# Performance work log

Measured on AMD Instinct MI355X. Metric: run time of the kernel, lower is better.

The kernel has to match this reference:

```python
import jax, jax.numpy as jnp
import numpy as np

B, N, D, H, E = 32, 512, 512, 8, 4
HD = D // H
EPS = 1e-3  # keras LayerNormalization default epsilon
NEG = -1e9  # keras Softmax masking additive constant


def _ln(x, g, b):
    m = jnp.mean(x, axis=-1, keepdims=True)
    v = jnp.mean(jnp.square(x - m), axis=-1, keepdims=True)
    return (x - m) * jax.lax.rsqrt(v + EPS) * g + b


def setup_inputs() -> dict:
    key = jax.random.key(0)
    ks = jax.random.split(key, 16)
    s = 0.02
    return {
        "x": jax.random.normal(ks[0], (B, N, D), jnp.float32),
        "mask": jax.random.randint(ks[1], (B, 1, N, N), 0, 2) > 0,
        "interaction": jax.random.normal(ks[2], (B, N, N, H), jnp.float32),
        "w_qkv": jax.random.normal(ks[3], (D, 3 * D), jnp.float32) * s,
        "b_qkv": jnp.zeros((3 * D,), jnp.float32),
        "w_out": jax.random.normal(ks[4], (D, D), jnp.float32) * s,
        "b_out": jnp.zeros((D,), jnp.float32),
        "w1": jax.random.normal(ks[5], (D, E * D), jnp.float32) * s,
        "b1": jnp.zeros((E * D,), jnp.float32),
        "w2": jax.random.normal(ks[6], (E * D, D), jnp.float32) * s,
        "b2": jnp.zeros((D,), jnp.float32),
        "g_pre": jnp.ones((D,), jnp.float32), "be_pre": jnp.zeros((D,), jnp.float32),
        "g_post": jnp.ones((D,), jnp.float32), "be_post": jnp.zeros((D,), jnp.float32),
        "g_ffn": jnp.ones((D,), jnp.float32), "be_ffn": jnp.zeros((D,), jnp.float32),
        "g_mid": jnp.ones((E * D,), jnp.float32), "be_mid": jnp.zeros((E * D,), jnp.float32),
    }


def reference(x, mask, interaction, w_qkv, b_qkv, w_out, b_out, w1, b1, w2, b2,
              g_pre, be_pre, g_post, be_post, g_ffn, be_ffn, g_mid, be_mid):
    # pre-LN MHSA
    h = _ln(x, g_pre, be_pre)
    qkv = h @ w_qkv + b_qkv                           # [B,N,3D]
    qkv = qkv.reshape(B, N, 3, H, HD)
    q, k, v = (jnp.transpose(qkv[:, :, i], (0, 2, 1, 3)) for i in range(3))  # [B,H,N,HD]
    scores = jnp.einsum('bhnd,bhmd->bhnm', q, k) / np.sqrt(HD).astype(np.float32)
    scores = scores + jnp.transpose(interaction, (0, 3, 1, 2))  # per-head additive bias
    scores = scores + (1.0 - mask.astype(scores.dtype)) * NEG   # keras Softmax mask semantics
    attn = jax.nn.softmax(scores, axis=-1)
    o = jnp.einsum('bhnm,bhmd->bhnd', attn, v)
    o = jnp.transpose(o, (0, 2, 1, 3)).reshape(B, N, D)
    o = o @ w_out + b_out
    attended = _ln(o, g_post, be_post) + x            # post-MHSA LN then residual
    # FFN with mid-LN
    f = _ln(attended, g_ffn, be_ffn)
    f = jax.nn.gelu(f @ w1 + b1, approximate=False)
    f = _ln(f, g_mid, be_mid)
    f = f @ w2 + b2
    return f + attended
```

## Files before the change

### kernel.cpp

```cpp
#include <hip/hip_runtime.h>
#include <hip/hip_bf16.h>
#include <math.h>

constexpr int CB = 32, CN = 512, CD = 512, CH = 8, CHD = 64;
constexpr float LN_EPS = 1e-3f;

typedef _Float16 half8 __attribute__((ext_vector_type(8)));
typedef float f32x4 __attribute__((ext_vector_type(4)));

__device__ __forceinline__ void async16(const void* g, void* l) {
    __builtin_amdgcn_global_load_lds((const __attribute__((address_space(1))) void*)g,
                                     (__attribute__((address_space(3))) void*)l, 16, 0, 0);
}

__global__ __launch_bounds__(256) void transpose_f16(const float* __restrict__ in,
                                                     _Float16* __restrict__ out,
                                                     int K, int N) {
    __shared__ float t[32][33];
    const int tx = threadIdx.x % 32, ty = threadIdx.x / 32;
    const int n0 = blockIdx.x * 32, k0 = blockIdx.y * 32;
#pragma unroll
    for (int i = 0; i < 4; ++i)
        t[ty + i * 8][tx] = in[(size_t)(k0 + ty + i * 8) * N + n0 + tx];
    __syncthreads();
#pragma unroll
    for (int i = 0; i < 4; ++i)
        out[(size_t)(n0 + ty + i * 8) * K + k0 + tx] = (_Float16)t[tx][ty + i * 8];
}

template<int WIDTH, bool IN_F16, bool OUT_F16, bool ADDRES>
__global__ __launch_bounds__(256) void ln2_kernel(const void* __restrict__ in_,
        const float* __restrict__ g, const float* __restrict__ be,
        const float* __restrict__ res, void* __restrict__ out_) {
    constexpr int NPL = WIDTH / 64;
    const int row = blockIdx.x * 4 + (threadIdx.x >> 6);
    const int lane = threadIdx.x & 63;
    const int c0 = lane * NPL;
    float v[NPL];
    if (IN_F16) {
        const _Float16* p = (const _Float16*)in_ + (size_t)row * WIDTH + c0;
#pragma unroll
        for (int i = 0; i < NPL / 8; ++i) {
            half8 u = *(const half8*)(p + i * 8);
#pragma unroll
            for (int j = 0; j < 8; ++j) v[i * 8 + j] = (float)u[j];
        }
    } else {
        const float* p = (const float*)in_ + (size_t)row * WIDTH + c0;
#pragma unroll
        for (int i = 0; i < NPL / 4; ++i) {
            float4 u = *(const float4*)(p + i * 4);
            v[i * 4 + 0] = u.x; v[i * 4 + 1] = u.y; v[i * 4 + 2] = u.z; v[i * 4 + 3] = u.w;
        }
    }
    float s1 = 0.f, s2 = 0.f;
#pragma unroll
    for (int i = 0; i < NPL; ++i) { s1 += v[i]; s2 += v[i] * v[i]; }
#pragma unroll
    for (int off = 1; off < 64; off <<= 1) { s1 += __shfl_xor(s1, off); s2 += __shfl_xor(s2, off); }
    const float mean = s1 * (1.0f / WIDTH);
    const float var = s2 * (1.0f / WIDTH) - mean * mean;
    const float rstd = rsqrtf(var + LN_EPS);

    float ov[NPL];
#pragma unroll
    for (int i = 0; i < NPL / 4; ++i) {
        float4 gv = *(const float4*)(g + c0 + i * 4);
        float4 bv = *(const float4*)(be + c0 + i * 4);
        ov[i * 4 + 0] = (v[i * 4 + 0] - mean) * rstd * gv.x + bv.x;
        ov[i * 4 + 1] = (v[i * 4 + 1] - mean) * rstd * gv.y + bv.y;
        ov[i * 4 + 2] = (v[i * 4 + 2] - mean) * rstd * gv.z + bv.z;
        ov[i * 4 + 3] = (v[i * 4 + 3] - mean) * rstd * gv.w + bv.w;
    }
    if (ADDRES) {
        const float* rp = res + (size_t)row * WIDTH + c0;
#pragma unroll
        for (int i = 0; i < NPL / 4; ++i) {
            float4 rv = *(const float4*)(rp + i * 4);
            ov[i * 4 + 0] += rv.x; ov[i * 4 + 1] += rv.y; ov[i * 4 + 2] += rv.z; ov[i * 4 + 3] += rv.w;
        }
    }
    if (OUT_F16) {
        _Float16* po = (_Float16*)out_ + (size_t)row * WIDTH + c0;
#pragma unroll
        for (int i = 0; i < NPL / 8; ++i) {
            half8 hv;
#pragma unroll
            for (int j = 0; j < 8; ++j) hv[j] = (_Float16)ov[i * 8 + j];
            *(half8*)(po + i * 8) = hv;
        }
    } else {
        float* po = (float*)out_ + (size_t)row * WIDTH + c0;
#pragma unroll
        for (int i = 0; i < NPL / 4; ++i) {
            float4 w = make_float4(ov[i * 4 + 0], ov[i * 4 + 1], ov[i * 4 + 2], ov[i * 4 + 3]);
            *(float4*)(po + i * 4) = w;
        }
    }
}

__global__ __launch_bounds__(256) void ln_post_ffn(const _Float16* __restrict__ o2,
        const float* __restrict__ x,
        const float* __restrict__ g_post, const float* __restrict__ be_post,
        const float* __restrict__ g_ffn, const float* __restrict__ be_ffn,
        float* __restrict__ attended, _Float16* __restrict__ f) {
    constexpr int NPL = 8;
    const int row = blockIdx.x * 4 + (threadIdx.x >> 6);
    const int lane = threadIdx.x & 63;
    const int c0 = lane * NPL;
    float v[NPL], xv[NPL];
    {
        half8 u = *(const half8*)(o2 + (size_t)row * CD + c0);
#pragma unroll
        for (int j = 0; j < 8; ++j) v[j] = (float)u[j];
        float4 a = *(const float4*)(x + (size_t)row * CD + c0);
        float4 b = *(const float4*)(x + (size_t)row * CD + c0 + 4);
        xv[0] = a.x; xv[1] = a.y; xv[2] = a.z; xv[3] = a.w;
        xv[4] = b.x; xv[5] = b.y; xv[6] = b.z; xv[7] = b.w;
    }
    float s1 = 0.f, s2 = 0.f;
#pragma unroll
    for (int i = 0; i < NPL; ++i) { s1 += v[i]; s2 += v[i] * v[i]; }
#pragma unroll
    for (int off = 1; off < 64; off <<= 1) { s1 += __shfl_xor(s1, off); s2 += __shfl_xor(s2, off); }
    float mean = s1 * (1.0f / CD);
    float rstd = rsqrtf(s2 * (1.0f / CD) - mean * mean + LN_EPS);
    float av[NPL];
#pragma unroll
    for (int i = 0; i < NPL; ++i)
        av[i] = (v[i] - mean) * rstd * g_post[c0 + i] + be_post[c0 + i] + xv[i];
    {
        float4 w0 = make_float4(av[0], av[1], av[2], av[3]);
        float4 w1 = make_float4(av[4], av[5], av[6], av[7]);
        *(float4*)(attended + (size_t)row * CD + c0) = w0;
        *(float4*)(attended + (size_t)row * CD + c0 + 4) = w1;
    }
    s1 = 0.f; s2 = 0.f;
#pragma unroll
    for (int i = 0; i < NPL; ++i) { s1 += av[i]; s2 += av[i] * av[i]; }
#pragma unroll
    for (int off = 1; off < 64; off <<= 1) { s1 += __shfl_xor(s1, off); s2 += __shfl_xor(s2, off); }
    mean = s1 * (1.0f / CD);
    rstd = rsqrtf(s2 * (1.0f / CD) - mean * mean + LN_EPS);
    half8 hv;
#pragma unroll
    for (int i = 0; i < NPL; ++i)
        hv[i] = (_Float16)((av[i] - mean) * rstd * g_ffn[c0 + i] + be_ffn[c0 + i]);
    *(half8*)(f + (size_t)row * CD + c0) = hv;
}

template<bool GELU, bool RES, bool OUT_F16>
__global__ __launch_bounds__(256) void gemm_f16(const _Float16* __restrict__ A,
        const _Float16* __restrict__ Wt, const float* __restrict__ bias,
        const float* __restrict__ res, void* __restrict__ Cout,
        int M, int N, int K) {
    __shared__ __align__(16) char As[16384];
    __shared__ __align__(16) char Bs[16384];
    const int tid = threadIdx.x;
    const int nbx = N >> 7;
    const int nwg = (M >> 7) * nbx;
    int gb = blockIdx.x;
    gb = (gb & 7) * (nwg >> 3) + (gb >> 3);
    const int by = gb / nbx, bx = gb % nbx;

    const int lane = tid & 63;
    const int wv = tid >> 6;
    const int rsub = lane >> 3;
    const int slot = lane & 7;
    const int chunk = slot ^ rsub;
    const _Float16* Abase = A + (size_t)(by * 128) * K + chunk * 8;
    const _Float16* Bbase = Wt + (size_t)(bx * 128) * K + chunk * 8;

    const int wm = wv >> 1, wn = wv & 1;
    const int lrow = lane & 15;
    const int lk = lane >> 4;
    const int xorv = lane & 7;
    const int aRowB = (wm * 64 + lrow) * 128;
    const int bRowB = (wn * 64 + lrow) * 128;

    f32x4 acc[4][4] = {};

    for (int k0 = 0; k0 < K; k0 += 64) {
#pragma unroll
        for (int t = 0; t < 4; ++t) {
            const int rowb = t * 32 + wv * 8;
            async16(Abase + (size_t)(rowb + rsub) * K + k0, As + rowb * 128);
            async16(Bbase + (size_t)(rowb + rsub) * K + k0, Bs + rowb * 128);
        }
        __syncthreads();
#pragma unroll
        for (int kk = 0; kk < 2; ++kk) {
            const int sa = ((kk * 4 + lk) ^ xorv) << 4;
            half8 af[4], bf[4];
#pragma unroll
            for (int mi = 0; mi < 4; ++mi) af[mi] = *(const half8*)(As + aRowB + mi * 2048 + sa);
#pragma unroll
            for (int ni = 0; ni < 4; ++ni) bf[ni] = *(const half8*)(Bs + bRowB + ni * 2048 + sa);
#pragma unroll
            for (int mi = 0; mi < 4; ++mi)
#pragma unroll
                for (int ni = 0; ni < 4; ++ni)
                    acc[mi][ni] = __builtin_amdgcn_mfma_f32_16x16x32_f16(af[mi], bf[ni], acc[mi][ni], 0, 0, 0);
        }
        __syncthreads();
    }

    const int lr4 = (lane >> 4) * 4;
    const int lc = lane & 15;
#pragma unroll
    for (int ni = 0; ni < 4; ++ni) {
        const int colg = bx * 128 + wn * 64 + ni * 16 + lc;
        const float bv = bias[colg];
#pragma unroll
        for (int mi = 0; mi < 4; ++mi) {
            const int rowg = by * 128 + wm * 64 + mi * 16 + lr4;
#pragma unroll
            for (int r = 0; r < 4; ++r) {
                float v = acc[mi][ni][r] + bv;
                if (GELU) v = 0.5f * v * (1.0f + erff(v * 0.70710678118654752440f));
                if (RES) v += res[(size_t)(rowg + r) * N + colg];
                if (OUT_F16) ((_Float16*)Cout)[(size_t)(rowg + r) * N + colg] = (_Float16)v;
                else ((float*)Cout)[(size_t)(rowg + r) * N + colg] = v;
            }
        }
    }
}

__global__ __launch_bounds__(256) void attn_mfma(
        const _Float16* __restrict__ qkv, const float* __restrict__ inter,
        const int* __restrict__ mask, _Float16* __restrict__ o) {
    const int bid = blockIdx.x;
    const int xcd = bid & 7;
    const int s = bid >> 3;
    const int h = s & 7;
    const int qt = (s >> 3) & 7;
    const int b = (s >> 6) * 8 + xcd;
    const int tid = threadIdx.x;
    const int lane = tid & 63;
    const int w = tid >> 6;
    const int l15 = lane & 15, l4 = lane >> 4;

    __shared__ __align__(16) char Qs[8192];
    __shared__ __align__(16) char Ks[8192];
    __shared__ __align__(16) char Vt[8192];
    __shared__ __align__(16) char Ps[8192];

    constexpr size_t QKVROW = 1536;
    {
        const _Float16* Qg = qkv + (size_t)(b * CN + qt * 64) * QKVROW + h * 64;
#pragma unroll
        for (int p = 0; p < 2; ++p) {
            const int f = tid + 256 * p;
            const int r = f >> 3, c = f & 7;
            half8 v = *(const half8*)(Qg + (size_t)r * QKVROW + c * 8);
            *(half8*)(Qs + r * 128 + ((c ^ (r & 7)) << 4)) = v;
        }
    }

    f32x4 acc_o[4] = {};
    float m_run[4] = {-3e38f, -3e38f, -3e38f, -3e38f};
    float l_run[4] = {0.f, 0.f, 0.f, 0.f};

    const int qg0 = qt * 64 + w * 16 + l4 * 4;
    const float* interB[4];
    const int* maskB[4];
#pragma unroll
    for (int r = 0; r < 4; ++r) {
        interB[r] = inter + ((size_t)(b * CN + qg0 + r) * CN) * CH + h;
        maskB[r]  = mask + (size_t)(b * CN + qg0 + r) * CN;
    }

    for (int mt = 0; mt < 8; ++mt) {
        __syncthreads();
        const _Float16* Kg = qkv + (size_t)(b * CN + mt * 64) * QKVROW + 512 + h * 64;
        const _Float16* Vg = Kg + 512;
#pragma unroll
        for (int p = 0; p < 2; ++p) {
            const int f = tid + 256 * p;
            const int r = f >> 3, c = f & 7;
            half8 kv = *(const half8*)(Kg + (size_t)r * QKVROW + c * 8);
            *(half8*)(Ks + r * 128 + ((c ^ (r & 7)) << 4)) = kv;
        }
#pragma unroll
        for (int p = 0; p < 2; ++p) {
            const int f = tid + 256 * p;
            const int m = f >> 3, dc = f & 7;
            half8 vv = *(const half8*)(Vg + (size_t)m * QKVROW + dc * 8);
            const int mc = m >> 3, mo = m & 7;
#pragma unroll
            for (int j = 0; j < 8; ++j) {
                const int d = dc * 8 + j;
                *(_Float16*)(Vt + d * 128 + ((mc ^ (d & 7)) << 4) + mo * 2) = vv[j];
            }
        }
        float iv[4][4];
#pragma unroll
        for (int r = 0; r < 4; ++r)
#pragma unroll
            for (int mi = 0; mi < 4; ++mi) {
                const int m = mt * 64 + mi * 16 + l15;
                const float bvv = interB[r][(size_t)m * CH];
                iv[r][mi] = bvv + (maskB[r][m] ? 0.f : -1e9f);
            }
        __syncthreads();

        f32x4 acc_s[4] = {};
#pragma unroll
        for (int step = 0; step < 2; ++step) {
            const int qrow = w * 16 + l15;
            const int ch = step * 4 + l4;
            half8 aq = *(const half8*)(Qs + qrow * 128 + ((ch ^ (qrow & 7)) << 4));
#pragma unroll
            for (int mi = 0; mi < 4; ++mi) {
                const int mrow = mi * 16 + l15;
                half8 bk = *(const half8*)(Ks + mrow * 128 + ((ch ^ (mrow & 7)) << 4));
                acc_s[mi] = __builtin_amdgcn_mfma_f32_16x16x32_f16(aq, bk, acc_s[mi], 0, 0, 0);
            }
        }
#pragma unroll
        for (int r = 0; r < 4; ++r) {
            float pv[4];
            float rmax = -3e38f;
#pragma unroll
            for (int mi = 0; mi < 4; ++mi) {
                float sv = acc_s[mi][r] * 0.125f + iv[r][mi];
                pv[mi] = sv;
                rmax = fmaxf(rmax, sv);
            }
#pragma unroll
            for (int off = 1; off < 16; off <<= 1) rmax = fmaxf(rmax, __shfl_xor(rmax, off));
            const float nm = fmaxf(m_run[r], rmax);
            const float fac = __expf(m_run[r] - nm);
            m_run[r] = nm;
            float ps = 0.f;
#pragma unroll
            for (int mi = 0; mi < 4; ++mi) { float e = __expf(pv[mi] - nm); pv[mi] = e; ps += e; }
#pragma unroll
            for (int off = 1; off < 16; off <<= 1) ps += __shfl_xor(ps, off);
            l_run[r] = l_run[r] * fac + ps;
#pragma unroll
            for (int di = 0; di < 4; ++di) acc_o[di][r] *= fac;
            const int qrow = w * 16 + l4 * 4 + r;
#pragma unroll
            for (int mi = 0; mi < 4; ++mi) {
                const int m = mi * 16 + l15;
                *(_Float16*)(Ps + qrow * 128 + (((m >> 3) ^ (qrow & 7)) << 4) + (m & 7) * 2) = (_Float16)pv[mi];
            }
        }
#pragma unroll
        for (int step = 0; step < 2; ++step) {
            const int qrow = w * 16 + l15;
            const int ch = step * 4 + l4;
            half8 ap = *(const half8*)(Ps + qrow * 128 + ((ch ^ (qrow & 7)) << 4));
#pragma unroll
            for (int di = 0; di < 4; ++di) {
                const int drow = di * 16 + l15;
                half8 bv = *(const half8*)(Vt + drow * 128 + ((ch ^ (drow & 7)) << 4));
                acc_o[di] = __builtin_amdgcn_mfma_f32_16x16x32_f16(ap, bv, acc_o[di], 0, 0, 0);
            }
        }
    }
    _Float16* orow = o + (size_t)(b * CN + qt * 64 + w * 16 + l4 * 4) * CD + h * 64 + l15;
#pragma unroll
    for (int r = 0; r < 4; ++r) {
        const float inv = 1.0f / l_run[r];
#pragma unroll
        for (int di = 0; di < 4; ++di)
            orow[(size_t)r * CD + di * 16] = (_Float16)(acc_o[di][r] * inv);
    }
}

extern "C" void kernel_launch(void* const* d_in, const int* in_sizes, int n_in,
                              void* d_out, int out_size, void* d_ws, size_t ws_size,
                              hipStream_t stream) {
    const float* x      = (const float*)d_in[0];
    const int*   mask   = (const int*)d_in[1];
    const float* inter  = (const float*)d_in[2];
    const float* w_qkv  = (const float*)d_in[3];
    const float* b_qkv  = (const float*)d_in[4];
    const float* w_out  = (const float*)d_in[5];
    const float* b_out  = (const float*)d_in[6];
    const float* w1     = (const float*)d_in[7];
    const float* b1     = (const float*)d_in[8];
    const float* w2     = (const float*)d_in[9];
    const float* b2     = (const float*)d_in[10];
    const float* g_pre  = (const float*)d_in[11];
    const float* be_pre = (const float*)d_in[12];
    const float* g_post = (const float*)d_in[13];
    const float* be_post= (const float*)d_in[14];
    const float* g_ffn  = (const float*)d_in[15];
    const float* be_ffn = (const float*)d_in[16];
    const float* g_mid  = (const float*)d_in[17];
    const float* be_mid = (const float*)d_in[18];
    float* out = (float*)d_out;

    char* ws = (char*)d_ws;
    const size_t MB = 1ull << 20;
    _Float16* wt_qkv = (_Float16*)(ws + 0 * MB);
    _Float16* wt_out = (_Float16*)(ws + 2 * MB);
    _Float16* wt_w1  = (_Float16*)(ws + 3 * MB);
    _Float16* wt_w2  = (_Float16*)(ws + 5 * MB);
    float*    attended = (float*)(ws + 8 * MB);
    _Float16* o2h    = (_Float16*)(ws + 40 * MB);
    _Float16* f1b    = (_Float16*)(ws + 64 * MB);
    _Float16* qkvb   = (_Float16*)(ws + 128 * MB);
    _Float16* hb     = (_Float16*)(ws + 176 * MB);
    _Float16* ob     = (_Float16*)(ws + 192 * MB);
    _Float16* fb     = (_Float16*)(ws + 208 * MB);

    const int M = CB * CN;

    transpose_f16<<<dim3(1536 / 32, 512 / 32), 256, 0, stream>>>(w_qkv, wt_qkv, 512, 1536);
    transpose_f16<<<dim3(512 / 32, 512 / 32), 256, 0, stream>>>(w_out, wt_out, 512, 512);
    transpose_f16<<<dim3(2048 / 32, 512 / 32), 256, 0, stream>>>(w1, wt_w1, 512, 2048);
    transpose_f16<<<dim3(512 / 32, 2048 / 32), 256, 0, stream>>>(w2, wt_w2, 2048, 512);

    ln2_kernel<512, false, true, false><<<M / 4, 256, 0, stream>>>(x, g_pre, be_pre, nullptr, hb);
    gemm_f16<false, false, true><<<(M / 128) * (1536 / 128), 256, 0, stream>>>(
        hb, wt_qkv, b_qkv, nullptr, qkvb, M, 1536, 512);
    attn_mfma<<<CB * 8 * 8, 256, 0, stream>>>(qkvb, inter, mask, ob);
    gemm_f16<false, false, true><<<(M / 128) * (512 / 128), 256, 0, stream>>>(
        ob, wt_out, b_out, nullptr, o2h, M, 512, 512);
    ln_post_ffn<<<M / 4, 256, 0, stream>>>(o2h, x, g_post, be_post, g_ffn, be_ffn, attended, fb);
    gemm_f16<true, false, true><<<(M / 128) * (2048 / 128), 256, 0, stream>>>(
        fb, wt_w1, b1, nullptr, f1b, M, 2048, 512);
    ln2_kernel<2048, true, true, false><<<M / 4, 256, 0, stream>>>(f1b, g_mid, be_mid, nullptr, f1b);
    gemm_f16<false, true, false><<<(M / 128) * (512 / 128), 256, 0, stream>>>(
        f1b, wt_w2, b2, attended, out, M, 512, 2048);
}
```

Before: 460.9 us.

## Transpose attention score MFMA so each lane owns one query row for softmax

The QK^T MFMA operands are swapped so the score tile comes out transposed: each lane holds 16 key scores for a single query row. Row max and sum then need only two cross-lane shuffles instead of four per row, mask values are read as int4 vectors, and P is written to LDS as packed half4 stores instead of scalar halves. The running rescale factors and the final normalisers are broadcast back to the output layout with shuffles. s_setprio is also raised around the MFMA blocks in both the GEMM and attention kernels to favour matrix issue across waves.

```diff
diff --git a/kernel.cpp b/kernel.cpp
--- a/kernel.cpp
+++ b/kernel.cpp
@@ -6,6 +6,7 @@
 constexpr float LN_EPS = 1e-3f;
 
 typedef _Float16 half8 __attribute__((ext_vector_type(8)));
+typedef _Float16 half4v __attribute__((ext_vector_type(4)));
 typedef float f32x4 __attribute__((ext_vector_type(4)));
 
 __device__ __forceinline__ void async16(const void* g, void* l) {
@@ -196,11 +197,13 @@
             for (int mi = 0; mi < 4; ++mi) af[mi] = *(const half8*)(As + aRowB + mi * 2048 + sa);
 #pragma unroll
             for (int ni = 0; ni < 4; ++ni) bf[ni] = *(const half8*)(Bs + bRowB + ni * 2048 + sa);
+            __builtin_amdgcn_s_setprio(1);
 #pragma unroll
             for (int mi = 0; mi < 4; ++mi)
 #pragma unroll
                 for (int ni = 0; ni < 4; ++ni)
                     acc[mi][ni] = __builtin_amdgcn_mfma_f32_16x16x32_f16(af[mi], bf[ni], acc[mi][ni], 0, 0, 0);
+            __builtin_amdgcn_s_setprio(0);
         }
         __syncthreads();
     }
@@ -258,17 +261,11 @@
     }
 
     f32x4 acc_o[4] = {};
-    float m_run[4] = {-3e38f, -3e38f, -3e38f, -3e38f};
-    float l_run[4] = {0.f, 0.f, 0.f, 0.f};
-
-    const int qg0 = qt * 64 + w * 16 + l4 * 4;
-    const float* interB[4];
-    const int* maskB[4];
-#pragma unroll
-    for (int r = 0; r < 4; ++r) {
-        interB[r] = inter + ((size_t)(b * CN + qg0 + r) * CN) * CH + h;
-        maskB[r]  = mask + (size_t)(b * CN + qg0 + r) * CN;
-    }
+    float m_run = -3e38f, l_run = 0.f;
+
+    const int q_sm = qt * 64 + w * 16 + l15;
+    const float* interB = inter + ((size_t)(b * CN + q_sm) * CN) * CH + h;
+    const int* maskB = mask + (size_t)(b * CN + q_sm) * CN;
 
     for (int mt = 0; mt < 8; ++mt) {
         __syncthreads();
@@ -295,13 +292,14 @@
         }
         float iv[4][4];
 #pragma unroll
-        for (int r = 0; r < 4; ++r)
-#pragma unroll
-            for (int mi = 0; mi < 4; ++mi) {
-                const int m = mt * 64 + mi * 16 + l15;
-                const float bvv = interB[r][(size_t)m * CH];
-                iv[r][mi] = bvv + (maskB[r][m] ? 0.f : -1e9f);
-            }
+        for (int mi = 0; mi < 4; ++mi) {
+            const int m0 = mt * 64 + mi * 16 + l4 * 4;
+            const int4 mv = *(const int4*)(maskB + m0);
+            iv[mi][0] = interB[(size_t)(m0 + 0) * CH] + (mv.x ? 0.f : -1e9f);
+            iv[mi][1] = interB[(size_t)(m0 + 1) * CH] + (mv.y ? 0.f : -1e9f);
+            iv[mi][2] = interB[(size_t)(m0 + 2) * CH] + (mv.z ? 0.f : -1e9f);
+            iv[mi][3] = interB[(size_t)(m0 + 3) * CH] + (mv.w ? 0.f : -1e9f);
+        }
         __syncthreads();
 
         f32x4 acc_s[4] = {};
@@ -309,42 +307,59 @@
         for (int step = 0; step < 2; ++step) {
             const int qrow = w * 16 + l15;
             const int ch = step * 4 + l4;
-            half8 aq = *(const half8*)(Qs + qrow * 128 + ((ch ^ (qrow & 7)) << 4));
+            half8 bq = *(const half8*)(Qs + qrow * 128 + ((ch ^ (qrow & 7)) << 4));
+            __builtin_amdgcn_s_setprio(1);
 #pragma unroll
             for (int mi = 0; mi < 4; ++mi) {
                 const int mrow = mi * 16 + l15;
-                half8 bk = *(const half8*)(Ks + mrow * 128 + ((ch ^ (mrow & 7)) << 4));
-                acc_s[mi] = __builtin_amdgcn_mfma_f32_16x16x32_f16(aq, bk, acc_s[mi], 0, 0, 0);
-            }
-        }
-#pragma unroll
-        for (int r = 0; r < 4; ++r) {
-            float pv[4];
-            float rmax = -3e38f;
+                half8 ak = *(const half8*)(Ks + mrow * 128 + ((ch ^ (mrow & 7)) << 4));
+                acc_s[mi] = __builtin_amdgcn_mfma_f32_16x16x32_f16(ak, bq, acc_s[mi], 0, 0, 0);
+            }
+            __builtin_amdgcn_s_setprio(0);
+        }
+        float sv[4][4];
+        float rmax = -3e38f;
+#pragma unroll
+        for (int mi = 0; mi < 4; ++mi)
+#pragma unroll
+            for (int r = 0; r < 4; ++r) {
+                const float t = acc_s[mi][r] * 0.125f + iv[mi][r];
+                sv[mi][r] = t;
+                rmax = fmaxf(rmax, t);
+            }
+        rmax = fmaxf(rmax, __shfl_xor(rmax, 16));
+        rmax = fmaxf(rmax, __shfl_xor(rmax, 32));
+        const float nm = fmaxf(m_run, rmax);
+        const float fac = __expf(m_run - nm);
+        m_run = nm;
+        float ps = 0.f;
+#pragma unroll
+        for (int mi = 0; mi < 4; ++mi)
+#pragma unroll
+            for (int r = 0; r < 4; ++r) {
+                const float e = __expf(sv[mi][r] - nm);
+                sv[mi][r] = e;
+                ps += e;
+            }
+        ps += __shfl_xor(ps, 16);
+        ps += __shfl_xor(ps, 32);
+        l_run = l_run * fac + ps;
+        float facO[4];
+#pragma unroll
+        for (int r = 0; r < 4; ++r) facO[r] = __shfl(fac, l4 * 4 + r);
+#pragma unroll
+        for (int di = 0; di < 4; ++di)
+#pragma unroll
+            for (int r = 0; r < 4; ++r) acc_o[di][r] *= facO[r];
+        {
+            const int qloc = w * 16 + l15;
 #pragma unroll
             for (int mi = 0; mi < 4; ++mi) {
-                float sv = acc_s[mi][r] * 0.125f + iv[r][mi];
-                pv[mi] = sv;
-                rmax = fmaxf(rmax, sv);
-            }
-#pragma unroll
-            for (int off = 1; off < 16; off <<= 1) rmax = fmaxf(rmax, __shfl_xor(rmax, off));
-            const float nm = fmaxf(m_run[r], rmax);
-            const float fac = __expf(m_run[r] - nm);
-            m_run[r] = nm;
-            float ps = 0.f;
-#pragma unroll
-            for (int mi = 0; mi < 4; ++mi) { float e = __expf(pv[mi] - nm); pv[mi] = e; ps += e; }
-#pragma unroll
-            for (int off = 1; off < 16; off <<= 1) ps += __shfl_xor(ps, off);
-            l_run[r] = l_run[r] * fac + ps;
-#pragma unroll
-            for (int di = 0; di < 4; ++di) acc_o[di][r] *= fac;
-            const int qrow = w * 16 + l4 * 4 + r;
-#pragma unroll
-            for (int mi = 0; mi < 4; ++mi) {
-                const int m = mi * 16 + l15;
-                *(_Float16*)(Ps + qrow * 128 + (((m >> 3) ^ (qrow & 7)) << 4) + (m & 7) * 2) = (_Float16)pv[mi];
+                half4v pk;
+#pragma unroll
+                for (int r = 0; r < 4; ++r) pk[r] = (_Float16)sv[mi][r];
+                const int c16 = (mi * 2 + (l4 >> 1)) ^ (qloc & 7);
+                *(half4v*)(Ps + qloc * 128 + c16 * 16 + (l4 & 1) * 8) = pk;
             }
         }
 #pragma unroll
@@ -352,21 +367,25 @@
             const int qrow = w * 16 + l15;
             const int ch = step * 4 + l4;
             half8 ap = *(const half8*)(Ps + qrow * 128 + ((ch ^ (qrow & 7)) << 4));
+            __builtin_amdgcn_s_setprio(1);
 #pragma unroll
             for (int di = 0; di < 4; ++di) {
                 const int drow = di * 16 + l15;
                 half8 bv = *(const half8*)(Vt + drow * 128 + ((ch ^ (drow & 7)) << 4));
                 acc_o[di] = __builtin_amdgcn_mfma_f32_16x16x32_f16(ap, bv, acc_o[di], 0, 0, 0);
             }
-        }
-    }
+            __builtin_amdgcn_s_setprio(0);
+        }
+    }
+    float invO[4];
+#pragma unroll
+    for (int r = 0; r < 4; ++r) invO[r] = 1.0f / __shfl(l_run, l4 * 4 + r);
     _Float16* orow = o + (size_t)(b * CN + qt * 64 + w * 16 + l4 * 4) * CD + h * 64 + l15;
 #pragma unroll
     for (int r = 0; r < 4; ++r) {
-        const float inv = 1.0f / l_run[r];
 #pragma unroll
         for (int di = 0; di < 4; ++di)
-            orow[(size_t)r * CD + di * 16] = (_Float16)(acc_o[di][r] * inv);
+            orow[(size_t)r * CD + di * 16] = (_Float16)(acc_o[di][r] * invO[r]);
     }
 }
 
```

New measurement: 606.6 us. 1.32x slower.

## Double-buffer K/V tiles in attention with async LDS loads for K

Applied to the files above, without the earlier changes.

The attention kernel now keeps two K and two V shared-memory buffers. While the current key tile is computed, it prefetches the next one: K is copied straight into LDS with global_load_lds, and V is loaded into registers and written transposed after the softmax. This cuts the loop to one barrier per tile and hides global load latency behind the MFMA and softmax work. The mask select is moved to the point of use so the raw bias and mask loads can be issued early. The cost is twice the K/V LDS footprint, which may lower occupancy, plus more live registers for the V prefetch and the mask values.

```diff
diff --git a/kernel.cpp b/kernel.cpp
--- a/kernel.cpp
+++ b/kernel.cpp
@@ -241,11 +241,19 @@
     const int l15 = lane & 15, l4 = lane >> 4;
 
     __shared__ __align__(16) char Qs[8192];
-    __shared__ __align__(16) char Ks[8192];
-    __shared__ __align__(16) char Vt[8192];
     __shared__ __align__(16) char Ps[8192];
+    __shared__ __align__(16) char Kb[2][8192];
+    __shared__ __align__(16) char Vb[2][8192];
 
     constexpr size_t QKVROW = 1536;
+    const _Float16* kvK = qkv + (size_t)(b * CN) * QKVROW + 512 + h * 64;
+
+    const int rsub = lane >> 3, slot = lane & 7;
+    const int chunkK = slot ^ rsub;
+    const int w16 = w * 16;
+    const int vm0 = tid >> 3, vm1 = vm0 + 32;
+    const int vdc = tid & 7;
+
     {
         const _Float16* Qg = qkv + (size_t)(b * CN + qt * 64) * QKVROW + h * 64;
 #pragma unroll
@@ -256,12 +264,27 @@
             *(half8*)(Qs + r * 128 + ((c ^ (r & 7)) << 4)) = v;
         }
     }
+    {
+        const _Float16* Kg = kvK;
+        async16(Kg + (size_t)(w16 + rsub) * QKVROW + chunkK * 8, Kb[0] + w16 * 128);
+        async16(Kg + (size_t)(w16 + 8 + rsub) * QKVROW + chunkK * 8, Kb[0] + (w16 + 8) * 128);
+        const _Float16* Vg = Kg + 512;
+        half8 v0 = *(const half8*)(Vg + (size_t)vm0 * QKVROW + vdc * 8);
+        half8 v1 = *(const half8*)(Vg + (size_t)vm1 * QKVROW + vdc * 8);
+#pragma unroll
+        for (int j = 0; j < 8; ++j) {
+            const int d = vdc * 8 + j;
+            *(_Float16*)(Vb[0] + d * 128 + (((vm0 >> 3) ^ (d & 7)) << 4) + (vm0 & 7) * 2) = v0[j];
+            *(_Float16*)(Vb[0] + d * 128 + (((vm1 >> 3) ^ (d & 7)) << 4) + (vm1 & 7) * 2) = v1[j];
+        }
+    }
+    __syncthreads();
 
     f32x4 acc_o[4] = {};
     float m_run[4] = {-3e38f, -3e38f, -3e38f, -3e38f};
     float l_run[4] = {0.f, 0.f, 0.f, 0.f};
 
-    const int qg0 = qt * 64 + w * 16 + l4 * 4;
+    const int qg0 = qt * 64 + w16 + l4 * 4;
     const float* interB[4];
     const int* maskB[4];
 #pragma unroll
@@ -270,50 +293,38 @@
         maskB[r]  = mask + (size_t)(b * CN + qg0 + r) * CN;
     }
 
-    for (int mt = 0; mt < 8; ++mt) {
-        __syncthreads();
-        const _Float16* Kg = qkv + (size_t)(b * CN + mt * 64) * QKVROW + 512 + h * 64;
-        const _Float16* Vg = Kg + 512;
-#pragma unroll
-        for (int p = 0; p < 2; ++p) {
-            const int f = tid + 256 * p;
-            const int r = f >> 3, c = f & 7;
-            half8 kv = *(const half8*)(Kg + (size_t)r * QKVROW + c * 8);
-            *(half8*)(Ks + r * 128 + ((c ^ (r & 7)) << 4)) = kv;
-        }
-#pragma unroll
-        for (int p = 0; p < 2; ++p) {
-            const int f = tid + 256 * p;
-            const int m = f >> 3, dc = f & 7;
-            half8 vv = *(const half8*)(Vg + (size_t)m * QKVROW + dc * 8);
-            const int mc = m >> 3, mo = m & 7;
-#pragma unroll
-            for (int j = 0; j < 8; ++j) {
-                const int d = dc * 8 + j;
-                *(_Float16*)(Vt + d * 128 + ((mc ^ (d & 7)) << 4) + mo * 2) = vv[j];
-            }
+    auto body = [&](char* KC, char* VC, char* KN, char* VN, int mt) {
+        if (mt != 7) {
+            const _Float16* KgN = kvK + (size_t)((mt + 1) * 64) * QKVROW;
+            async16(KgN + (size_t)(w16 + rsub) * QKVROW + chunkK * 8, KN + w16 * 128);
+            async16(KgN + (size_t)(w16 + 8 + rsub) * QKVROW + chunkK * 8, KN + (w16 + 8) * 128);
+        }
+        half8 v0, v1;
+        if (mt != 7) {
+            const _Float16* VgN = kvK + (size_t)((mt + 1) * 64) * QKVROW + 512;
+            v0 = *(const half8*)(VgN + (size_t)vm0 * QKVROW + vdc * 8);
+            v1 = *(const half8*)(VgN + (size_t)vm1 * QKVROW + vdc * 8);
         }
         float iv[4][4];
+        int mvv[4][4];
 #pragma unroll
         for (int r = 0; r < 4; ++r)
 #pragma unroll
             for (int mi = 0; mi < 4; ++mi) {
                 const int m = mt * 64 + mi * 16 + l15;
-                const float bvv = interB[r][(size_t)m * CH];
-                iv[r][mi] = bvv + (maskB[r][m] ? 0.f : -1e9f);
-            }
-        __syncthreads();
-
+                iv[r][mi] = interB[r][(size_t)m * CH];
+                mvv[r][mi] = maskB[r][m];
+            }
         f32x4 acc_s[4] = {};
 #pragma unroll
         for (int step = 0; step < 2; ++step) {
-            const int qrow = w * 16 + l15;
+            const int qrow = w16 + l15;
             const int ch = step * 4 + l4;
             half8 aq = *(const half8*)(Qs + qrow * 128 + ((ch ^ (qrow & 7)) << 4));
 #pragma unroll
             for (int mi = 0; mi < 4; ++mi) {
                 const int mrow = mi * 16 + l15;
-                half8 bk = *(const half8*)(Ks + mrow * 128 + ((ch ^ (mrow & 7)) << 4));
+                half8 bk = *(const half8*)(KC + mrow * 128 + ((ch ^ (mrow & 7)) << 4));
                 acc_s[mi] = __builtin_amdgcn_mfma_f32_16x16x32_f16(aq, bk, acc_s[mi], 0, 0, 0);
             }
         }
@@ -323,7 +334,7 @@
             float rmax = -3e38f;
 #pragma unroll
             for (int mi = 0; mi < 4; ++mi) {
-                float sv = acc_s[mi][r] * 0.125f + iv[r][mi];
+                float sv = acc_s[mi][r] * 0.125f + iv[r][mi] + (mvv[r][mi] ? 0.f : -1e9f);
                 pv[mi] = sv;
                 rmax = fmaxf(rmax, sv);
             }
@@ -340,27 +351,42 @@
             l_run[r] = l_run[r] * fac + ps;
 #pragma unroll
             for (int di = 0; di < 4; ++di) acc_o[di][r] *= fac;
-            const int qrow = w * 16 + l4 * 4 + r;
+            const int qrow = w16 + l4 * 4 + r;
 #pragma unroll
             for (int mi = 0; mi < 4; ++mi) {
                 const int m = mi * 16 + l15;
                 *(_Float16*)(Ps + qrow * 128 + (((m >> 3) ^ (qrow & 7)) << 4) + (m & 7) * 2) = (_Float16)pv[mi];
             }
         }
+        if (mt != 7) {
+#pragma unroll
+            for (int j = 0; j < 8; ++j) {
+                const int d = vdc * 8 + j;
+                *(_Float16*)(VN + d * 128 + (((vm0 >> 3) ^ (d & 7)) << 4) + (vm0 & 7) * 2) = v0[j];
+                *(_Float16*)(VN + d * 128 + (((vm1 >> 3) ^ (d & 7)) << 4) + (vm1 & 7) * 2) = v1[j];
+            }
+        }
 #pragma unroll
         for (int step = 0; step < 2; ++step) {
-            const int qrow = w * 16 + l15;
+            const int qrow = w16 + l15;
             const int ch = step * 4 + l4;
             half8 ap = *(const half8*)(Ps + qrow * 128 + ((ch ^ (qrow & 7)) << 4));
 #pragma unroll
             for (int di = 0; di < 4; ++di) {
                 const int drow = di * 16 + l15;
-                half8 bv = *(const half8*)(Vt + drow * 128 + ((ch ^ (drow & 7)) << 4));
+                half8 bv = *(const half8*)(VC + drow * 128 + ((ch ^ (drow & 7)) << 4));
                 acc_o[di] = __builtin_amdgcn_mfma_f32_16x16x32_f16(ap, bv, acc_o[di], 0, 0, 0);
             }
         }
-    }
-    _Float16* orow = o + (size_t)(b * CN + qt * 64 + w * 16 + l4 * 4) * CD + h * 64 + l15;
+        __syncthreads();
+    };
+
+    for (int it = 0; it < 4; ++it) {
+        body(Kb[0], Vb[0], Kb[1], Vb[1], it * 2);
+        body(Kb[1], Vb[1], Kb[0], Vb[0], it * 2 + 1);
+    }
+
+    _Float16* orow = o + (size_t)(b * CN + qt * 64 + w16 + l4 * 4) * CD + h * 64 + l15;
 #pragma unroll
     for (int r = 0; r < 4; ++r) {
         const float inv = 1.0f / l_run[r];
```

After: 470.8 us. 1.02x slower.

## Process four heads per attention block with vectorized bias loads

Applied to the files above, without the earlier changes.

Restructures the attention kernel so each block handles four heads for one query tile. The per-head additive bias is read as a float4 across heads in one coalesced access, and mask reads are shared across those heads, cutting redundant global traffic on the large interaction tensor. Q is held in registers pre-scaled by the softmax scale, K tiles are loaded via async global-to-LDS, and the bias+mask are stored in fp16 with a smaller mask constant. This raises register and LDS use and reduces precision of the bias term.

```diff
diff --git a/kernel.cpp b/kernel.cpp
--- a/kernel.cpp
+++ b/kernel.cpp
@@ -6,6 +6,7 @@
 constexpr float LN_EPS = 1e-3f;
 
 typedef _Float16 half8 __attribute__((ext_vector_type(8)));
+typedef _Float16 half4v __attribute__((ext_vector_type(4)));
 typedef float f32x4 __attribute__((ext_vector_type(4)));
 
 __device__ __forceinline__ void async16(const void* g, void* l) {
@@ -226,147 +227,162 @@
     }
 }
 
-__global__ __launch_bounds__(256) void attn_mfma(
+__global__ __launch_bounds__(256, 2) void attn_mfma(
         const _Float16* __restrict__ qkv, const float* __restrict__ inter,
         const int* __restrict__ mask, _Float16* __restrict__ o) {
     const int bid = blockIdx.x;
     const int xcd = bid & 7;
-    const int s = bid >> 3;
-    const int h = s & 7;
-    const int qt = (s >> 3) & 7;
-    const int b = (s >> 6) * 8 + xcd;
+    const int rest = bid >> 3;
+    const int b = (rest & 3) * 8 + xcd;
+    const int qt = (rest >> 2) & 7;
+    const int hq = rest >> 5;
+    const int h0 = hq * 4;
     const int tid = threadIdx.x;
     const int lane = tid & 63;
     const int w = tid >> 6;
     const int l15 = lane & 15, l4 = lane >> 4;
-
-    __shared__ __align__(16) char Qs[8192];
-    __shared__ __align__(16) char Ks[8192];
-    __shared__ __align__(16) char Vt[8192];
+    const int w16 = w * 16;
+
+    __shared__ __align__(16) char Ks[4][8192];
+    __shared__ __align__(16) char Vt[4][8192];
     __shared__ __align__(16) char Ps[8192];
 
-    constexpr size_t QKVROW = 1536;
+    constexpr size_t QROW = 1536;
+    const int rsub = lane >> 3, slot = lane & 7;
+    const int chunkK = slot ^ rsub;
+
+    half8 q0[4], q1[4];
     {
-        const _Float16* Qg = qkv + (size_t)(b * CN + qt * 64) * QKVROW + h * 64;
-#pragma unroll
-        for (int p = 0; p < 2; ++p) {
-            const int f = tid + 256 * p;
-            const int r = f >> 3, c = f & 7;
-            half8 v = *(const half8*)(Qg + (size_t)r * QKVROW + c * 8);
-            *(half8*)(Qs + r * 128 + ((c ^ (r & 7)) << 4)) = v;
-        }
-    }
-
-    f32x4 acc_o[4] = {};
-    float m_run[4] = {-3e38f, -3e38f, -3e38f, -3e38f};
-    float l_run[4] = {0.f, 0.f, 0.f, 0.f};
-
-    const int qg0 = qt * 64 + w * 16 + l4 * 4;
+        const _Float16* qg = qkv + (size_t)(b * CN + qt * 64 + w16 + l15) * QROW + h0 * 64;
+#pragma unroll
+        for (int hh = 0; hh < 4; ++hh) {
+            q0[hh] = *(const half8*)(qg + hh * 64 + l4 * 8);
+            q1[hh] = *(const half8*)(qg + hh * 64 + 32 + l4 * 8);
+#pragma unroll
+            for (int j = 0; j < 8; ++j) {
+                q0[hh][j] = q0[hh][j] * (_Float16)0.125f;
+                q1[hh][j] = q1[hh][j] * (_Float16)0.125f;
+            }
+        }
+    }
+
+    const int qg0 = qt * 64 + w16 + l4 * 4;
     const float* interB[4];
     const int* maskB[4];
 #pragma unroll
     for (int r = 0; r < 4; ++r) {
-        interB[r] = inter + ((size_t)(b * CN + qg0 + r) * CN) * CH + h;
+        interB[r] = inter + ((size_t)(b * CN + qg0 + r) * CN) * CH + h0;
         maskB[r]  = mask + (size_t)(b * CN + qg0 + r) * CN;
     }
 
+    f32x4 acc_o[4][4] = {};
+    float m_run[4][4], l_run[4][4];
+#pragma unroll
+    for (int hh = 0; hh < 4; ++hh)
+#pragma unroll
+        for (int r = 0; r < 4; ++r) { m_run[hh][r] = -3e38f; l_run[hh][r] = 0.f; }
+
     for (int mt = 0; mt < 8; ++mt) {
-        __syncthreads();
-        const _Float16* Kg = qkv + (size_t)(b * CN + mt * 64) * QKVROW + 512 + h * 64;
-        const _Float16* Vg = Kg + 512;
-#pragma unroll
-        for (int p = 0; p < 2; ++p) {
-            const int f = tid + 256 * p;
-            const int r = f >> 3, c = f & 7;
-            half8 kv = *(const half8*)(Kg + (size_t)r * QKVROW + c * 8);
-            *(half8*)(Ks + r * 128 + ((c ^ (r & 7)) << 4)) = kv;
-        }
-#pragma unroll
-        for (int p = 0; p < 2; ++p) {
-            const int f = tid + 256 * p;
-            const int m = f >> 3, dc = f & 7;
-            half8 vv = *(const half8*)(Vg + (size_t)m * QKVROW + dc * 8);
-            const int mc = m >> 3, mo = m & 7;
-#pragma unroll
-            for (int j = 0; j < 8; ++j) {
-                const int d = dc * 8 + j;
-                *(_Float16*)(Vt + d * 128 + ((mc ^ (d & 7)) << 4) + mo * 2) = vv[j];
-            }
-        }
-        float iv[4][4];
+        half4v iv16[4][4];
 #pragma unroll
         for (int r = 0; r < 4; ++r)
 #pragma unroll
             for (int mi = 0; mi < 4; ++mi) {
                 const int m = mt * 64 + mi * 16 + l15;
-                const float bvv = interB[r][(size_t)m * CH];
-                iv[r][mi] = bvv + (maskB[r][m] ? 0.f : -1e9f);
-            }
+                const float4 f = *(const float4*)(interB[r] + (size_t)m * CH);
+                const float add = maskB[r][m] ? 0.f : -30000.f;
+                half4v hv;
+                hv[0] = (_Float16)(f.x + add); hv[1] = (_Float16)(f.y + add);
+                hv[2] = (_Float16)(f.z + add); hv[3] = (_Float16)(f.w + add);
+                iv16[r][mi] = hv;
+            }
+        const _Float16* Kg = qkv + (size_t)(b * CN + mt * 64) * QROW + 512 + (h0 + w) * 64;
+#pragma unroll
+        for (int i = 0; i < 8; ++i)
+            async16(Kg + (size_t)(i * 8 + rsub) * QROW + chunkK * 8, Ks[w] + i * 1024);
+        const _Float16* Vg = Kg + 512;
+#pragma unroll
+        for (int k = 0; k < 8; ++k) {
+            const int m = (lane >> 3) + k * 8;
+            half8 vv = *(const half8*)(Vg + (size_t)m * QROW + (lane & 7) * 8);
+#pragma unroll
+            for (int j = 0; j < 8; ++j) {
+                const int d = (lane & 7) * 8 + j;
+                *(_Float16*)(Vt[w] + d * 128 + (((m >> 3) ^ (d & 7)) << 4) + (m & 7) * 2) = vv[j];
+            }
+        }
         __syncthreads();
 
-        f32x4 acc_s[4] = {};
-#pragma unroll
-        for (int step = 0; step < 2; ++step) {
-            const int qrow = w * 16 + l15;
-            const int ch = step * 4 + l4;
-            half8 aq = *(const half8*)(Qs + qrow * 128 + ((ch ^ (qrow & 7)) << 4));
-#pragma unroll
-            for (int mi = 0; mi < 4; ++mi) {
-                const int mrow = mi * 16 + l15;
-                half8 bk = *(const half8*)(Ks + mrow * 128 + ((ch ^ (mrow & 7)) << 4));
-                acc_s[mi] = __builtin_amdgcn_mfma_f32_16x16x32_f16(aq, bk, acc_s[mi], 0, 0, 0);
-            }
-        }
+#pragma unroll
+        for (int hh = 0; hh < 4; ++hh) {
+            f32x4 acc_s[4] = {};
+#pragma unroll
+            for (int step = 0; step < 2; ++step) {
+                const half8 aq = step == 0 ? q0[hh] : q1[hh];
+                const int ch = step * 4 + l4;
+#pragma unroll
+                for (int mi = 0; mi < 4; ++mi) {
+                    const int mrow = mi * 16 + l15;
+                    half8 bk = *(const half8*)(Ks[hh] + mrow * 128 + ((ch ^ (mrow & 7)) << 4));
+                    acc_s[mi] = __builtin_amdgcn_mfma_f32_16x16x32_f16(aq, bk, acc_s[mi], 0, 0, 0);
+                }
+            }
+#pragma unroll
+            for (int r = 0; r < 4; ++r) {
+                float pv[4];
+                float rmax = -3e38f;
+#pragma unroll
+                for (int mi = 0; mi < 4; ++mi) {
+                    float sv = acc_s[mi][r] + (float)iv16[r][mi][hh];
+                    pv[mi] = sv;
+                    rmax = fmaxf(rmax, sv);
+                }
+#pragma unroll
+                for (int off = 1; off < 16; off <<= 1) rmax = fmaxf(rmax, __shfl_xor(rmax, off));
+                const float nm = fmaxf(m_run[hh][r], rmax);
+                const float fac = __expf(m_run[hh][r] - nm);
+                m_run[hh][r] = nm;
+                float ps = 0.f;
+#pragma unroll
+                for (int mi = 0; mi < 4; ++mi) { float e = __expf(pv[mi] - nm); pv[mi] = e; ps += e; }
+#pragma unroll
+                for (int off = 1; off < 16; off <<= 1) ps += __shfl_xor(ps, off);
+                l_run[hh][r] = l_run[hh][r] * fac + ps;
+#pragma unroll
+                for (int di = 0; di < 4; ++di) acc_o[hh][di][r] *= fac;
+                const int qrow = w16 + l4 * 4 + r;
+#pragma unroll
+                for (int mi = 0; mi < 4; ++mi) {
+                    const int m = mi * 16 + l15;
+                    *(_Float16*)(Ps + qrow * 128 + (((m >> 3) ^ (qrow & 7)) << 4) + (m & 7) * 2) = (_Float16)pv[mi];
+                }
+            }
+#pragma unroll
+            for (int step = 0; step < 2; ++step) {
+                const int qrow = w16 + l15;
+                const int ch = step * 4 + l4;
+                half8 ap = *(const half8*)(Ps + qrow * 128 + ((ch ^ (qrow & 7)) << 4));
+#pragma unroll
+                for (int di = 0; di < 4; ++di) {
+                    const int drow = di * 16 + l15;
+                    half8 bv = *(const half8*)(Vt[hh] + drow * 128 + ((ch ^ (drow & 7)) << 4));
+                    acc_o[hh][di] = __builtin_amdgcn_mfma_f32_16x16x32_f16(ap, bv, acc_o[hh][di], 0, 0, 0);
+                }
+            }
+        }
+        __syncthreads();
+    }
+
+#pragma unroll
+    for (int hh = 0; hh < 4; ++hh) {
+        _Float16* orow = o + (size_t)(b * CN + qt * 64 + w16 + l4 * 4) * CD + (h0 + hh) * 64 + l15;
 #pragma unroll
         for (int r = 0; r < 4; ++r) {
-            float pv[4];
-            float rmax = -3e38f;
-#pragma unroll
-            for (int mi = 0; mi < 4; ++mi) {
-                float sv = acc_s[mi][r] * 0.125f + iv[r][mi];
-                pv[mi] = sv;
-                rmax = fmaxf(rmax, sv);
-            }
-#pragma unroll
-            for (int off = 1; off < 16; off <<= 1) rmax = fmaxf(rmax, __shfl_xor(rmax, off));
-            const float nm = fmaxf(m_run[r], rmax);
-            const float fac = __expf(m_run[r] - nm);
-            m_run[r] = nm;
-            float ps = 0.f;
-#pragma unroll
-            for (int mi = 0; mi < 4; ++mi) { float e = __expf(pv[mi] - nm); pv[mi] = e; ps += e; }
-#pragma unroll
-            for (int off = 1; off < 16; off <<= 1) ps += __shfl_xor(ps, off);
-            l_run[r] = l_run[r] * fac + ps;
-#pragma unroll
-            for (int di = 0; di < 4; ++di) acc_o[di][r] *= fac;
-            const int qrow = w * 16 + l4 * 4 + r;
-#pragma unroll
-            for (int mi = 0; mi < 4; ++mi) {
-                const int m = mi * 16 + l15;
-                *(_Float16*)(Ps + qrow * 128 + (((m >> 3) ^ (qrow & 7)) << 4) + (m & 7) * 2) = (_Float16)pv[mi];
-            }
-        }
-#pragma unroll
-        for (int step = 0; step < 2; ++step) {
-            const int qrow = w * 16 + l15;
-            const int ch = step * 4 + l4;
-            half8 ap = *(const half8*)(Ps + qrow * 128 + ((ch ^ (qrow & 7)) << 4));
-#pragma unroll
-            for (int di = 0; di < 4; ++di) {
-                const int drow = di * 16 + l15;
-                half8 bv = *(const half8*)(Vt + drow * 128 + ((ch ^ (drow & 7)) << 4));
-                acc_o[di] = __builtin_amdgcn_mfma_f32_16x16x32_f16(ap, bv, acc_o[di], 0, 0, 0);
-            }
-        }
-    }
-    _Float16* orow = o + (size_t)(b * CN + qt * 64 + w * 16 + l4 * 4) * CD + h * 64 + l15;
-#pragma unroll
-    for (int r = 0; r < 4; ++r) {
-        const float inv = 1.0f / l_run[r];
-#pragma unroll
-        for (int di = 0; di < 4; ++di)
-            orow[(size_t)r * CD + di * 16] = (_Float16)(acc_o[di][r] * inv);
+            const float inv = 1.0f / l_run[hh][r];
+#pragma unroll
+            for (int di = 0; di < 4; ++di)
+                orow[(size_t)r * CD + di * 16] = (_Float16)(acc_o[hh][di][r] * inv);
+        }
     }
 }
 
@@ -418,7 +434,7 @@
     ln2_kernel<512, false, true, false><<<M / 4, 256, 0, stream>>>(x, g_pre, be_pre, nullptr, hb);
     gemm_f16<false, false, true><<<(M / 128) * (1536 / 128), 256, 0, stream>>>(
         hb, wt_qkv, b_qkv, nullptr, qkvb, M, 1536, 512);
-    attn_mfma<<<CB * 8 * 8, 256, 0, stream>>>(qkvb, inter, mask, ob);
+    attn_mfma<<<512, 256, 0, stream>>>(qkvb, inter, mask, ob);
     gemm_f16<false, false, true><<<(M / 128) * (512 / 128), 256, 0, stream>>>(
         ob, wt_out, b_out, nullptr, o2h, M, 512, 512);
     ln_post_ffn<<<M / 4, 256, 0, stream>>>(o2h, x, g_post, be_post, g_ffn, be_ffn, attended, fb);
```

Measured after the change: 479.2 us. 1.04x slower.
